# Optimization experiments

Hardware: AMD Instinct MI355X
Metric: run time of the kernel (lower is better)

## Reference

```python
import jax, jax.numpy as jnp
import numpy as np

N = 100000          # nodes
E = 1600000         # edges
D_IN = 128
HID = 256
N_CLASSES = 10
N_GRAPHS = 64


def gcn_conv(x, src, dst, W, b, n_nodes):
    """PyG GCNConv: add self-loops, symmetric deg^{-1/2} normalization, x@W, scatter-add."""
    h = x @ W  # [N, out]
    loop = jnp.arange(n_nodes, dtype=src.dtype)
    src2 = jnp.concatenate([src, loop])
    dst2 = jnp.concatenate([dst, loop])
    deg = jax.ops.segment_sum(jnp.ones(src2.shape[0], x.dtype), dst2, num_segments=n_nodes)
    dinv = jax.lax.rsqrt(deg)  # deg >= 1 thanks to self-loops
    norm = dinv[src2] * dinv[dst2]  # [E+N]
    msg = norm[:, None] * h[src2]   # [E+N, out]
    return jax.ops.segment_sum(msg, dst2, num_segments=n_nodes) + b


def setup_inputs() -> dict:
    key = jax.random.key(0)
    ks = jax.random.split(key, 12)
    x = jax.random.normal(ks[0], (N, D_IN), dtype=jnp.float32)
    edge_index = jax.random.randint(ks[1], (2, E), 0, N, dtype=jnp.int64)
    batch = jnp.sort(jax.random.randint(ks[2], (N,), 0, N_GRAPHS, dtype=jnp.int64))
    def glorot(k, shape):
        lim = float(np.sqrt(6.0 / (shape[0] + shape[1])))
        return jax.random.uniform(k, shape, jnp.float32, -lim, lim)
    W1 = glorot(ks[3], (D_IN, HID));  b1 = jnp.zeros((HID,), jnp.float32)
    W2 = glorot(ks[4], (HID, HID));   b2 = jnp.zeros((HID,), jnp.float32)
    Wf1 = glorot(ks[5], (HID, HID));  bf1 = jnp.zeros((HID,), jnp.float32)
    Wf2 = glorot(ks[6], (HID, N_CLASSES)); bf2 = jnp.zeros((N_CLASSES,), jnp.float32)
    return {"x": x, "edge_index": edge_index, "batch": batch,
            "W1": W1, "b1": b1, "W2": W2, "b2": b2,
            "Wf1": Wf1, "bf1": bf1, "Wf2": Wf2, "bf2": bf2}


def reference(x, edge_index, batch, W1, b1, W2, b2, Wf1, bf1, Wf2, bf2):
    src, dst = edge_index[0], edge_index[1]
    h = jax.nn.relu(gcn_conv(x, src, dst, W1, b1, N))
    h = jax.nn.relu(gcn_conv(h, src, dst, W2, b2, N))
    # global mean pool over graph ids
    summed = jax.ops.segment_sum(h, batch, num_segments=N_GRAPHS)  # [G, HID]
    counts = jax.ops.segment_sum(jnp.ones((N,), h.dtype), batch, num_segments=N_GRAPHS)
    pooled = summed / jnp.maximum(counts, 1.0)[:, None]
    z = jax.nn.relu(pooled @ Wf1 + bf1)
    alpha = jax.nn.softplus(z @ Wf2 + bf2) + 0.001
    return alpha
```

## Files before the change

### kernel.cpp

```cpp
#include <hip/hip_runtime.h>
#include <math.h>

#define NN   100000
#define NE   1600000
#define DIN  128
#define HID  256
#define NG   64
#define NCLS 10

#define NBLK 128
#define EPB  (NE / NBLK)
#define NBUK 512
#define NPB  196
#define NHIST (NBUK * NBLK)
#define NBR  ((NN + 127) / 128)

using bf16x8 = __attribute__((ext_vector_type(8))) short;
using f32x4  = __attribute__((ext_vector_type(4))) float;
using f32x2  = __attribute__((ext_vector_type(2))) float;
using u32x2  = __attribute__((ext_vector_type(2))) unsigned int;

static __device__ __forceinline__ unsigned short f2bf(float f) {
    unsigned u = __float_as_uint(f);
    u += 0x7fff + ((u >> 16) & 1);
    return (unsigned short)(u >> 16);
}

static __device__ __forceinline__ unsigned char f32_to_fp8(float f) {
    float a = fminf(fabsf(f), 448.f);
    unsigned bits = __float_as_uint(a * 0x1p-120f);
    bits += 0x7ffff + ((bits >> 20) & 1);
    unsigned e4 = (bits >> 20) & 0x7f;
    return (unsigned char)(e4 | (f < 0.f ? 0x80u : 0u));
}
#if __has_builtin(__builtin_amdgcn_cvt_pk_f32_fp8)
#define HAVE_CVT_FP8 1
#endif
static __device__ __forceinline__ void fp8x4_to_f32(unsigned u, float* f) {
#ifdef HAVE_CVT_FP8
    f32x2 lo = __builtin_amdgcn_cvt_pk_f32_fp8((int)u, false);
    f32x2 hi = __builtin_amdgcn_cvt_pk_f32_fp8((int)u, true);
    f[0] = lo[0]; f[1] = lo[1]; f[2] = hi[0]; f[3] = hi[1];
#else
#pragma unroll
    for (int k = 0; k < 4; ++k) {
        unsigned b = (u >> (8 * k)) & 0xffu;
        unsigned bits = ((b & 0x80u) << 24) | ((b & 0x7fu) << 20);
        f[k] = __uint_as_float(bits) * 0x1p+120f;
    }
#endif
}
static __device__ __forceinline__ int4 fp8x8_to_bf16x8(unsigned lo, unsigned hi) {
    float f[8];
    fp8x4_to_f32(lo, f);
    fp8x4_to_f32(hi, f + 4);
    int4 r;
    r.x = (int)((__float_as_uint(f[0]) >> 16) | (__float_as_uint(f[1]) & 0xffff0000u));
    r.y = (int)((__float_as_uint(f[2]) >> 16) | (__float_as_uint(f[3]) & 0xffff0000u));
    r.z = (int)((__float_as_uint(f[4]) >> 16) | (__float_as_uint(f[5]) & 0xffff0000u));
    r.w = (int)((__float_as_uint(f[6]) >> 16) | (__float_as_uint(f[7]) & 0xffff0000u));
    return r;
}


__global__ __launch_bounds__(256) void k_hist(const int* __restrict__ dst,
                                              int* __restrict__ histg) {
    __shared__ int h[NBUK];
    const int t = threadIdx.x;
    for (int i = t; i < NBUK; i += 256) h[i] = 0;
    __syncthreads();
    const int e0 = blockIdx.x * EPB, e1 = e0 + EPB;
    for (int e = e0 + t; e < e1; e += 256)
        atomicAdd(&h[(unsigned)__builtin_nontemporal_load(&dst[e]) / NPB], 1);
    __syncthreads();
    for (int i = t; i < NBUK; i += 256)
        histg[i * NBLK + blockIdx.x] = h[i];
}

__global__ __launch_bounds__(256) void k_bsum2(const int* __restrict__ d,
                                               int* __restrict__ bsum) {
    __shared__ int sd[256];
    int t = threadIdx.x;
    const int4 v = *(const int4*)&d[blockIdx.x * 1024 + t * 4];
    sd[t] = v.x + v.y + v.z + v.w;
    __syncthreads();
    for (int off = 128; off > 0; off >>= 1) {
        if (t < off) sd[t] += sd[t + off];
        __syncthreads();
    }
    if (t == 0) bsum[blockIdx.x] = sd[0];
}

__global__ void k_scanb2(const int* __restrict__ bsum, int* __restrict__ boff,
                         const int* __restrict__ batch, float* __restrict__ countsf) {
    __shared__ int tmp[64];
    int t = threadIdx.x;
    int v = bsum[t];
    tmp[t] = v; __syncthreads();
    for (int off = 1; off < 64; off <<= 1) {
        int u = (t >= off) ? tmp[t - off] : 0;
        __syncthreads();
        tmp[t] += u;
        __syncthreads();
    }
    boff[t] = tmp[t] - v;
    int g = t;
    int lo = 0, hi = NN;
    while (lo < hi) { int mid = (lo + hi) >> 1; if (batch[mid] < g) lo = mid + 1; else hi = mid; }
    int lb = lo;
    lo = 0; hi = NN;
    while (lo < hi) { int mid = (lo + hi) >> 1; if (batch[mid] <= g) lo = mid + 1; else hi = mid; }
    countsf[g] = (float)(lo - lb);
}

__global__ __launch_bounds__(256) void k_offs2(int* __restrict__ d,
                                               const int* __restrict__ boff) {
    __shared__ int ts[256];
    int t = threadIdx.x;
    int base = blockIdx.x * 1024 + t * 4;
    int4 v = *(const int4*)&d[base];
    int s = v.x + v.y + v.z + v.w;
    ts[t] = s; __syncthreads();
    for (int off = 1; off < 256; off <<= 1) {
        int u = (t >= off) ? ts[t - off] : 0;
        __syncthreads();
        ts[t] += u;
        __syncthreads();
    }
    int run = ts[t] - s + boff[blockIdx.x];
    int4 o;
    o.x = run; run += v.x;
    o.y = run; run += v.y;
    o.z = run; run += v.z;
    o.w = run; run += v.w;
    *(int4*)&d[base] = o;
}

__global__ __launch_bounds__(256) void k_scatter(const int* __restrict__ src,
                                                 const int* __restrict__ dst,
                                                 const int* __restrict__ offg,
                                                 unsigned* __restrict__ pairs) {
    __shared__ int cur[NBUK];
    const int t = threadIdx.x;
    for (int i = t; i < NBUK; i += 256) cur[i] = offg[i * NBLK + blockIdx.x];
    __syncthreads();
    const int e0 = blockIdx.x * EPB, e1 = e0 + EPB;
    for (int e = e0 + t; e < e1; e += 256) {
        int d = __builtin_nontemporal_load(&dst[e]);
        int sv = __builtin_nontemporal_load(&src[e]);
        int b = (unsigned)d / NPB;
        int li = d - b * NPB;
        unsigned pk = ((unsigned)li << 24) | (unsigned)sv;
        int p = atomicAdd(&cur[b], 1);
        __builtin_nontemporal_store(pk, &pairs[p]);
    }
}

__global__ __launch_bounds__(256) void k_csr(const unsigned* __restrict__ pairs,
                                             const int* __restrict__ offg,
                                             int* __restrict__ csr,
                                             int* __restrict__ deg,
                                             float* __restrict__ dinv,
                                             int* __restrict__ offs) {
    __shared__ int cnt[NPB];
    __shared__ int loff[256];
    __shared__ int cur[NPB];
    const int b = blockIdx.x, t = threadIdx.x;
    const int s     = offg[b * NBLK];
    const int e_end = (b == NBUK - 1) ? NE : offg[(b + 1) * NBLK];
    const int nb0   = b * NPB;
    const int nnod  = min(NPB, NN - nb0);
    if (t < NPB) cnt[t] = 0;
    __syncthreads();
    for (int e = s + t; e < e_end; e += 256)
        atomicAdd(&cnt[pairs[e] >> 24], 1);
    __syncthreads();
    int v = (t < NPB) ? cnt[t] : 0;
    loff[t] = v;
    __syncthreads();
    for (int off = 1; off < 256; off <<= 1) {
        int u = (t >= off) ? loff[t - off] : 0;
        __syncthreads();
        loff[t] += u;
        __syncthreads();
    }
    int myoff = loff[t] - v;
    __syncthreads();
    loff[t] = myoff;
    if (t < NPB) cur[t] = 0;
    __syncthreads();
    if (t < nnod) {
        int node = nb0 + t;
        int dg = cnt[t];
        deg[node]  = dg;
        dinv[node] = rsqrtf((float)(dg + 1));
        offs[node] = s + myoff;
    }
    for (int e = s + t; e < e_end; e += 256) {
        unsigned pk = pairs[e];
        int li = pk >> 24;
        int p = atomicAdd(&cur[li], 1);
        csr[s + loff[li] + p] = (int)(pk & 0xffffffu);
    }
}


#define XQ (NN * 32)

__global__ void k_cast_all(const float* __restrict__ x, const float* __restrict__ dinv,
                           unsigned char* __restrict__ xs8,
                           const float* __restrict__ W1, unsigned short* __restrict__ Wt1,
                           const float* __restrict__ W2, unsigned short* __restrict__ Wt2) {
    int i = blockIdx.x * blockDim.x + threadIdx.x;
    if (i < XQ) {
        int nd = i >> 5;
        int q  = i & 31;
        float dv = dinv[nd];
        const float4 v = *(const float4*)&x[(size_t)nd * DIN + q * 4];
        uchar4 o;
        o.x = f32_to_fp8(v.x * dv); o.y = f32_to_fp8(v.y * dv);
        o.z = f32_to_fp8(v.z * dv); o.w = f32_to_fp8(v.w * dv);
        *(uchar4*)&xs8[(size_t)nd * DIN + q * 4] = o;
        return;
    }
    int j = i - XQ;
    if (j < DIN * HID) {
        int k = j >> 8, nc = j & 255;
        Wt1[nc * DIN + k] = f2bf(W1[j]);
    } else if (j < (DIN + HID) * HID) {
        int jj = j - DIN * HID;
        int k = jj >> 8, nc = jj & 255;
        Wt2[nc * HID + k] = f2bf(W2[jj]);
    }
}


template <int MODE>
__global__ __launch_bounds__(256) void k_gemm_mfma(const unsigned char* __restrict__ A8,
                                                   const unsigned short* __restrict__ Wt,
                                                   const float* __restrict__ dinv,
                                                   const float* __restrict__ bias,
                                                   void* __restrict__ outp,
                                                   const int* __restrict__ batch,
                                                   int M, int K) {
    __shared__ unsigned short As[128 * 40];
    __shared__ unsigned short Bs[128 * 40];
    __shared__ float psum[4][128];
    __shared__ int gloc[128];
    const int t = threadIdx.x;
    const int lane = t & 63;
    const int wid = t >> 6;
    const int wr = wid >> 1, wc = wid & 1;
    const int bm = blockIdx.x * 128, bn = blockIdx.y * 128;
    const int lr = lane & 15;
    const int ko = (lane >> 4) << 3;

    f32x4 acc[4][4] = {};

    const int r = t >> 2;
    const int kq = (t & 3) << 3;

    int g0 = 0, gend = 0;
    if (MODE == 2) {
        g0 = batch[bm];
        gend = batch[min(bm + 127, M - 1)];
        for (int i = t; i < 4 * 128; i += 256) ((float*)psum)[i] = 0.f;
        if (t < 128) gloc[t] = (bm + t < M) ? min(batch[bm + t] - g0, 3) : 0;
    }

    for (int kk = 0; kk < K; kk += 32) {
#pragma unroll
        for (int h = 0; h < 128; h += 64) {
            int row = bm + r + h;
            int4 o = make_int4(0, 0, 0, 0);
            if (row < M) {
                u32x2 v = *(const u32x2*)&A8[(size_t)row * K + kk + kq];
                o = fp8x8_to_bf16x8(v.x, v.y);
            }
            *(int4*)&As[(r + h) * 40 + kq] = o;
        }
#pragma unroll
        for (int h = 0; h < 128; h += 64) {
            int nrow = bn + r + h;
            int4 v = *(const int4*)&Wt[(size_t)nrow * K + kk + kq];
            *(int4*)&Bs[(r + h) * 40 + kq] = v;
        }
        __syncthreads();
        bf16x8 af[4], bfr[4];
#pragma unroll
        for (int mf = 0; mf < 4; ++mf)
            af[mf] = *(const bf16x8*)&As[(wr * 64 + mf * 16 + lr) * 40 + ko];
#pragma unroll
        for (int nf = 0; nf < 4; ++nf)
            bfr[nf] = *(const bf16x8*)&Bs[(wc * 64 + nf * 16 + lr) * 40 + ko];
#pragma unroll
        for (int mf = 0; mf < 4; ++mf)
#pragma unroll
            for (int nf = 0; nf < 4; ++nf)
                acc[mf][nf] = __builtin_amdgcn_mfma_f32_16x16x32_bf16(af[mf], bfr[nf], acc[mf][nf], 0, 0, 0);
        __syncthreads();
    }

    if (MODE == 1) {
        unsigned char* out8 = (unsigned char*)outp;
#pragma unroll
        for (int mf = 0; mf < 4; ++mf) {
#pragma unroll
            for (int b = 0; b < 4; ++b) {
                int row = bm + wr * 64 + mf * 16 + (lane >> 4) * 4 + b;
                if (row >= M) continue;
                float dv = dinv[row];
#pragma unroll
                for (int nf = 0; nf < 4; ++nf) {
                    int col = bn + wc * 64 + nf * 16 + lr;
                    float v = fmaxf(acc[mf][nf][b] + bias[col], 0.f);
                    out8[(size_t)row * HID + col] = f32_to_fp8(dv * v);
                }
            }
        }
    } else {
        const int q4 = (lane >> 4) << 2;
        if (gend == g0) {
#pragma unroll
            for (int nf = 0; nf < 4; ++nf) {
                const int lcol = wc * 64 + nf * 16 + lr;
                const float bb = bias[bn + lcol];
                float rsum = 0.f;
#pragma unroll
                for (int mf = 0; mf < 4; ++mf)
#pragma unroll
                    for (int b = 0; b < 4; ++b) {
                        int lrow = wr * 64 + mf * 16 + q4 + b;
                        if (bm + lrow < M) rsum += fmaxf(acc[mf][nf][b] + bb, 0.f);
                    }
                rsum += __shfl_xor(rsum, 16);
                rsum += __shfl_xor(rsum, 32);
                if ((lane >> 4) == 0) atomicAdd(&psum[0][lcol], rsum);
            }
        } else {
#pragma unroll
            for (int nf = 0; nf < 4; ++nf) {
                const int lcol = wc * 64 + nf * 16 + lr;
                const float bb = bias[bn + lcol];
                float run = 0.f; int gcur = 0;
#pragma unroll
                for (int mf = 0; mf < 4; ++mf) {
#pragma unroll
                    for (int b = 0; b < 4; ++b) {
                        int lrow = wr * 64 + mf * 16 + q4 + b;
                        if (bm + lrow < M) {
                            int gl = gloc[lrow];
                            float v = fmaxf(acc[mf][nf][b] + bb, 0.f);
                            if (gl != gcur) {
                                if (run != 0.f) atomicAdd(&psum[gcur][lcol], run);
                                run = 0.f; gcur = gl;
                            }
                            run += v;
                        }
                    }
                }
                if (run != 0.f) atomicAdd(&psum[gcur][lcol], run);
            }
        }
        __syncthreads();
        float* scratch = (float*)outp;
        size_t base = ((size_t)blockIdx.x * 2 + blockIdx.y) * 512;
        for (int i = t; i < 512; i += 256)
            __builtin_nontemporal_store(((const float*)psum)[i], &scratch[base + i]);
    }
}


__global__ __launch_bounds__(128) void k_reduce(const float* __restrict__ scratch,
                                                const int* __restrict__ batch,
                                                float* __restrict__ pooled) {
    const int g = blockIdx.x >> 1, by = blockIdx.x & 1;
    const int t = threadIdx.x;
    int lo = 0, hi = NN;
    while (lo < hi) { int mid = (lo + hi) >> 1; if (batch[mid] < g) lo = mid + 1; else hi = mid; }
    int s = lo;
    lo = s; hi = NN;
    while (lo < hi) { int mid = (lo + hi) >> 1; if (batch[mid] <= g) lo = mid + 1; else hi = mid; }
    int e = lo;
    float sum = 0.f;
    if (e > s) {
        int bx0 = s >> 7, bx1 = (e - 1) >> 7;
        for (int bx = bx0; bx <= bx1; ++bx) {
            int gl = min(g - batch[bx << 7], 3);
            sum += scratch[((size_t)bx * 2 + by) * 512 + gl * 128 + t];
        }
    }
    pooled[g * HID + by * 128 + t] = sum;
}


__global__ __launch_bounds__(256) void k_agg256(const unsigned char* __restrict__ hs,
                                                const int* __restrict__ csr,
                                                const int* __restrict__ offs,
                                                const int* __restrict__ deg,
                                                const float* __restrict__ dinv,
                                                unsigned char* __restrict__ out, int n) {
    int wid = threadIdx.x >> 6, lane = threadIdx.x & 63;
    int node = blockIdx.x * 4 + wid;
    if (node >= n) return;
    int c = lane << 2;
    float a0, a1, a2, a3;
    {
        unsigned u = *(const unsigned*)&hs[(size_t)node * HID + c];
        float f[4]; fp8x4_to_f32(u, f);
        a0 = f[0]; a1 = f[1]; a2 = f[2]; a3 = f[3];
    }
    int s0 = offs[node], cnt = deg[node];
    for (int base = 0; base < cnt; base += 64) {
        int nb = min(64, cnt - base);
        int idx = (lane < nb) ? __builtin_nontemporal_load(&csr[s0 + base + lane]) : 0;
        int i = 0;
        for (; i + 8 <= nb; i += 8) {
            unsigned v[8];
#pragma unroll
            for (int k = 0; k < 8; ++k) {
                int j = __shfl(idx, i + k);
                v[k] = *(const unsigned*)&hs[(size_t)j * HID + c];
            }
#pragma unroll
            for (int k = 0; k < 8; ++k) {
                float f[4]; fp8x4_to_f32(v[k], f);
                a0 += f[0]; a1 += f[1]; a2 += f[2]; a3 += f[3];
            }
        }
        for (; i + 4 <= nb; i += 4) {
            unsigned v[4];
#pragma unroll
            for (int k = 0; k < 4; ++k) {
                int j = __shfl(idx, i + k);
                v[k] = *(const unsigned*)&hs[(size_t)j * HID + c];
            }
#pragma unroll
            for (int k = 0; k < 4; ++k) {
                float f[4]; fp8x4_to_f32(v[k], f);
                a0 += f[0]; a1 += f[1]; a2 += f[2]; a3 += f[3];
            }
        }
        for (; i < nb; ++i) {
            int j = __shfl(idx, i);
            unsigned u = *(const unsigned*)&hs[(size_t)j * HID + c];
            float f[4]; fp8x4_to_f32(u, f);
            a0 += f[0]; a1 += f[1]; a2 += f[2]; a3 += f[3];
        }
    }
    float dv = dinv[node];
    uchar4 r;
    r.x = f32_to_fp8(dv * a0); r.y = f32_to_fp8(dv * a1);
    r.z = f32_to_fp8(dv * a2); r.w = f32_to_fp8(dv * a3);
    *(uchar4*)&out[(size_t)node * HID + c] = r;
}


__global__ __launch_bounds__(256) void k_agg128(const unsigned char* __restrict__ xs,
                                                const int* __restrict__ csr,
                                                const int* __restrict__ offs,
                                                const int* __restrict__ deg,
                                                const float* __restrict__ dinv,
                                                unsigned char* __restrict__ out, int n) {
    int wid = threadIdx.x >> 6, lane = threadIdx.x & 63;
    int node = blockIdx.x * 4 + wid;
    if (node >= n) return;
    int half = lane >> 5, l32 = lane & 31;
    int c = l32 << 2;
    float a0 = 0.f, a1 = 0.f, a2 = 0.f, a3 = 0.f;
    if (half == 0) {
        unsigned u = *(const unsigned*)&xs[(size_t)node * DIN + c];
        float f[4]; fp8x4_to_f32(u, f);
        a0 = f[0]; a1 = f[1]; a2 = f[2]; a3 = f[3];
    }
    int s0 = offs[node], cnt = deg[node];
    for (int base = 0; base < cnt; base += 64) {
        int nb = min(64, cnt - base);
        int idx = (lane < nb) ? __builtin_nontemporal_load(&csr[s0 + base + lane]) : 0;
        int i = 0;
        for (; i + 8 <= nb; i += 8) {
            unsigned v[4];
#pragma unroll
            for (int k = 0; k < 4; ++k) {
                int j = __shfl(idx, i + 2 * k + half);
                v[k] = *(const unsigned*)&xs[(size_t)j * DIN + c];
            }
#pragma unroll
            for (int k = 0; k < 4; ++k) {
                float f[4]; fp8x4_to_f32(v[k], f);
                a0 += f[0]; a1 += f[1]; a2 += f[2]; a3 += f[3];
            }
        }
        for (; i < nb; i += 2) {
            int e = i + half;
            int j = __shfl(idx, e < nb ? e : 0);
            if (e < nb) {
                unsigned u = *(const unsigned*)&xs[(size_t)j * DIN + c];
                float f[4]; fp8x4_to_f32(u, f);
                a0 += f[0]; a1 += f[1]; a2 += f[2]; a3 += f[3];
            }
        }
    }
    a0 += __shfl_xor(a0, 32);
    a1 += __shfl_xor(a1, 32);
    a2 += __shfl_xor(a2, 32);
    a3 += __shfl_xor(a3, 32);
    if (half == 0) {
        float dv = dinv[node];
        uchar4 r;
        r.x = f32_to_fp8(dv * a0); r.y = f32_to_fp8(dv * a1);
        r.z = f32_to_fp8(dv * a2); r.w = f32_to_fp8(dv * a3);
        *(uchar4*)&out[(size_t)node * DIN + c] = r;
    }
}


__global__ __launch_bounds__(256) void k_mlp(const float* __restrict__ pooled,
                                             const float* __restrict__ countsf,
                                             const float* __restrict__ Wf1,
                                             const float* __restrict__ bf1,
                                             const float* __restrict__ Wf2,
                                             const float* __restrict__ bf2,
                                             float* __restrict__ out) {
    __shared__ float p[HID];
    __shared__ float z[HID];
    int g = blockIdx.x, t = threadIdx.x;
    float cnt = fmaxf(countsf[g], 1.0f);
    p[t] = pooled[g * HID + t] / cnt;
    __syncthreads();
    float accz = bf1[t];
    for (int k = 0; k < HID; ++k)
        accz = fmaf(p[k], Wf1[k * HID + t], accz);
    z[t] = fmaxf(accz, 0.f);
    __syncthreads();
    if (t < NCLS) {
        float o = bf2[t];
        for (int k = 0; k < HID; ++k)
            o = fmaf(z[k], Wf2[k * NCLS + t], o);
        float sp = fmaxf(o, 0.f) + log1pf(expf(-fabsf(o)));
        out[g * NCLS + t] = sp + 0.001f;
    }
}


extern "C" void kernel_launch(void* const* d_in, const int* in_sizes, int n_in,
                              void* d_out, int out_size, void* d_ws, size_t ws_size,
                              hipStream_t stream) {
    const float* x     = (const float*)d_in[0];
    const int*   ei    = (const int*)d_in[1];
    const int*   batch = (const int*)d_in[2];
    const float* W1    = (const float*)d_in[3];
    const float* b1    = (const float*)d_in[4];
    const float* W2    = (const float*)d_in[5];
    const float* b2    = (const float*)d_in[6];
    const float* Wf1   = (const float*)d_in[7];
    const float* bf1   = (const float*)d_in[8];
    const float* Wf2   = (const float*)d_in[9];
    const float* bf2   = (const float*)d_in[10];
    float* out = (float*)d_out;

    const int* srcv = ei;
    const int* dstv = ei + NE;

    char* p = (char*)d_ws;
    auto take = [&](size_t bytes) -> char* {
        char* q = p; p += (bytes + 255) & ~(size_t)255; return q;
    };
    char* big0 = take((size_t)NN * HID * 2);
    char* big1 = take((size_t)NN * HID * 2);
    unsigned char*  xs8 = (unsigned char*)big0;
    unsigned char*  xa8 = (unsigned char*)(big0 + (size_t)NN * DIN);
    unsigned char*  h8  = (unsigned char*)big1;
    unsigned char*  r8  = (unsigned char*)big0;
    float* scratch = (float*)(big1 + (size_t)NN * HID);
    unsigned* pairs = (unsigned*)big1;
    unsigned short* wt1  = (unsigned short*)take((size_t)DIN * HID * 2);
    unsigned short* wt2  = (unsigned short*)take((size_t)HID * HID * 2);
    int*   histg   = (int*)take((size_t)NHIST * 4);
    int*   bsum    = (int*)take(64 * 4);
    int*   boff    = (int*)take(64 * 4);
    int*   deg     = (int*)take((size_t)NN * 4);
    int*   offs    = (int*)take((size_t)NN * 4);
    int*   csr     = (int*)take((size_t)NE * 4);
    float* dinv    = (float*)take((size_t)NN * 4);
    float* pooled  = (float*)take((size_t)NG * HID * 4);
    float* countsf = (float*)take((size_t)NG * 4);

    k_hist<<<NBLK, 256, 0, stream>>>(dstv, histg);
    k_bsum2<<<64, 256, 0, stream>>>(histg, bsum);
    k_scanb2<<<1, 64, 0, stream>>>(bsum, boff, batch, countsf);
    k_offs2<<<64, 256, 0, stream>>>(histg, boff);
    k_scatter<<<NBLK, 256, 0, stream>>>(srcv, dstv, histg, pairs);
    k_csr<<<NBUK, 256, 0, stream>>>(pairs, histg, csr, deg, dinv, offs);

    int cast_total = XQ + (DIN + HID) * HID;
    k_cast_all<<<(cast_total + 255) / 256, 256, 0, stream>>>(x, dinv, xs8, W1, wt1, W2, wt2);

    dim3 gg(NBR, HID / 128);
    k_agg128<<<(NN + 3) / 4, 256, 0, stream>>>(xs8, csr, offs, deg, dinv, xa8, NN);
    k_gemm_mfma<1><<<gg, 256, 0, stream>>>(xa8, wt1, dinv, b1, (void*)h8, batch, NN, DIN);
    k_agg256<<<(NN + 3) / 4, 256, 0, stream>>>(h8, csr, offs, deg, dinv, r8, NN);
    k_gemm_mfma<2><<<gg, 256, 0, stream>>>(r8, wt2, dinv, b2, (void*)scratch, batch, NN, HID);
    k_reduce<<<2 * NG, 128, 0, stream>>>(scratch, batch, pooled);

    k_mlp<<<NG, 256, 0, stream>>>(pooled, countsf, Wf1, bf1, Wf2, bf2, out);
}
```

Baseline: 339.1 us.

## Widen GEMM block tile to full 256 columns with K-step 64

The GEMM block now covers 128 rows by all 256 output columns using 512 threads (8 waves), instead of two 128x128 blocks per row tile. The fp8 A tile is loaded and converted once per row block rather than twice, and the K loop steps by 64 with two MFMA sub-steps, halving the number of barriers. The pooled scratch layout is changed to 1024 floats per row block, and k_reduce is updated to match. This trades fewer blocks and more LDS per block (larger B tile) against lower occupancy.

```diff
diff --git a/kernel.cpp b/kernel.cpp
--- a/kernel.cpp
+++ b/kernel.cpp
@@ -19,6 +19,7 @@
 using f32x4  = __attribute__((ext_vector_type(4))) float;
 using f32x2  = __attribute__((ext_vector_type(2))) float;
 using u32x2  = __attribute__((ext_vector_type(2))) unsigned int;
+using u32x4  = __attribute__((ext_vector_type(4))) unsigned int;
 
 static __device__ __forceinline__ unsigned short f2bf(float f) {
     unsigned u = __float_as_uint(f);
@@ -236,68 +237,70 @@
 
 
 template <int MODE>
-__global__ __launch_bounds__(256) void k_gemm_mfma(const unsigned char* __restrict__ A8,
+__global__ __launch_bounds__(512) void k_gemm_mfma(const unsigned char* __restrict__ A8,
                                                    const unsigned short* __restrict__ Wt,
                                                    const float* __restrict__ dinv,
                                                    const float* __restrict__ bias,
                                                    void* __restrict__ outp,
                                                    const int* __restrict__ batch,
                                                    int M, int K) {
-    __shared__ unsigned short As[128 * 40];
-    __shared__ unsigned short Bs[128 * 40];
-    __shared__ float psum[4][128];
+    __shared__ unsigned short As[128 * 72];
+    __shared__ unsigned short Bs[256 * 72];
+    __shared__ float psum[4][256];
     __shared__ int gloc[128];
     const int t = threadIdx.x;
     const int lane = t & 63;
     const int wid = t >> 6;
-    const int wr = wid >> 1, wc = wid & 1;
-    const int bm = blockIdx.x * 128, bn = blockIdx.y * 128;
+    const int wr = wid & 1, wc = wid >> 1;
+    const int bm = blockIdx.x * 128;
     const int lr = lane & 15;
     const int ko = (lane >> 4) << 3;
 
     f32x4 acc[4][4] = {};
 
-    const int r = t >> 2;
-    const int kq = (t & 3) << 3;
+    const int arow = t >> 2;
+    const int akq  = (t & 3) << 4;
+    const int brow = t >> 1;
+    const int bkq  = (t & 1) << 5;
 
     int g0 = 0, gend = 0;
     if (MODE == 2) {
         g0 = batch[bm];
         gend = batch[min(bm + 127, M - 1)];
-        for (int i = t; i < 4 * 128; i += 256) ((float*)psum)[i] = 0.f;
+        for (int i = t; i < 4 * 256; i += 512) ((float*)psum)[i] = 0.f;
         if (t < 128) gloc[t] = (bm + t < M) ? min(batch[bm + t] - g0, 3) : 0;
     }
 
-    for (int kk = 0; kk < K; kk += 32) {
-#pragma unroll
-        for (int h = 0; h < 128; h += 64) {
-            int row = bm + r + h;
-            int4 o = make_int4(0, 0, 0, 0);
-            if (row < M) {
-                u32x2 v = *(const u32x2*)&A8[(size_t)row * K + kk + kq];
-                o = fp8x8_to_bf16x8(v.x, v.y);
-            }
-            *(int4*)&As[(r + h) * 40 + kq] = o;
-        }
-#pragma unroll
-        for (int h = 0; h < 128; h += 64) {
-            int nrow = bn + r + h;
-            int4 v = *(const int4*)&Wt[(size_t)nrow * K + kk + kq];
-            *(int4*)&Bs[(r + h) * 40 + kq] = v;
-        }
-        __syncthreads();
-        bf16x8 af[4], bfr[4];
-#pragma unroll
-        for (int mf = 0; mf < 4; ++mf)
-            af[mf] = *(const bf16x8*)&As[(wr * 64 + mf * 16 + lr) * 40 + ko];
-#pragma unroll
-        for (int nf = 0; nf < 4; ++nf)
-            bfr[nf] = *(const bf16x8*)&Bs[(wc * 64 + nf * 16 + lr) * 40 + ko];
-#pragma unroll
-        for (int mf = 0; mf < 4; ++mf)
+    for (int kk = 0; kk < K; kk += 64) {
+        {
+            int row = bm + arow;
+            u32x4 v; v.x = v.y = v.z = v.w = 0u;
+            if (row < M) v = *(const u32x4*)&A8[(size_t)row * K + kk + akq];
+            *(int4*)&As[arow * 72 + akq]     = fp8x8_to_bf16x8(v.x, v.y);
+            *(int4*)&As[arow * 72 + akq + 8] = fp8x8_to_bf16x8(v.z, v.w);
+        }
+        {
+            const unsigned short* wsrc = &Wt[(size_t)brow * K + kk + bkq];
+#pragma unroll
+            for (int q = 0; q < 4; ++q)
+                *(int4*)&Bs[brow * 72 + bkq + q * 8] = *(const int4*)&wsrc[q * 8];
+        }
+        __syncthreads();
+#pragma unroll
+        for (int ks = 0; ks < 64; ks += 32) {
+            bf16x8 af[4], bfr[4];
+#pragma unroll
+            for (int mf = 0; mf < 4; ++mf)
+                af[mf] = *(const bf16x8*)&As[(wr * 64 + mf * 16 + lr) * 72 + ks + ko];
 #pragma unroll
             for (int nf = 0; nf < 4; ++nf)
-                acc[mf][nf] = __builtin_amdgcn_mfma_f32_16x16x32_bf16(af[mf], bfr[nf], acc[mf][nf], 0, 0, 0);
+                bfr[nf] = *(const bf16x8*)&Bs[(wc * 64 + nf * 16 + lr) * 72 + ks + ko];
+#pragma unroll
+            for (int mf = 0; mf < 4; ++mf)
+#pragma unroll
+                for (int nf = 0; nf < 4; ++nf)
+                    acc[mf][nf] = __builtin_amdgcn_mfma_f32_16x16x32_bf16(af[mf], bfr[nf], acc[mf][nf], 0, 0, 0);
+        }
         __syncthreads();
     }
 
@@ -312,7 +315,7 @@
                 float dv = dinv[row];
 #pragma unroll
                 for (int nf = 0; nf < 4; ++nf) {
-                    int col = bn + wc * 64 + nf * 16 + lr;
+                    int col = wc * 64 + nf * 16 + lr;
                     float v = fmaxf(acc[mf][nf][b] + bias[col], 0.f);
                     out8[(size_t)row * HID + col] = f32_to_fp8(dv * v);
                 }
@@ -324,7 +327,7 @@
 #pragma unroll
             for (int nf = 0; nf < 4; ++nf) {
                 const int lcol = wc * 64 + nf * 16 + lr;
-                const float bb = bias[bn + lcol];
+                const float bb = bias[lcol];
                 float rsum = 0.f;
 #pragma unroll
                 for (int mf = 0; mf < 4; ++mf)
@@ -341,7 +344,7 @@
 #pragma unroll
             for (int nf = 0; nf < 4; ++nf) {
                 const int lcol = wc * 64 + nf * 16 + lr;
-                const float bb = bias[bn + lcol];
+                const float bb = bias[lcol];
                 float run = 0.f; int gcur = 0;
 #pragma unroll
                 for (int mf = 0; mf < 4; ++mf) {
@@ -364,8 +367,8 @@
         }
         __syncthreads();
         float* scratch = (float*)outp;
-        size_t base = ((size_t)blockIdx.x * 2 + blockIdx.y) * 512;
-        for (int i = t; i < 512; i += 256)
+        size_t base = (size_t)blockIdx.x * 1024;
+        for (int i = t; i < 1024; i += 512)
             __builtin_nontemporal_store(((const float*)psum)[i], &scratch[base + i]);
     }
 }
@@ -376,6 +379,7 @@
                                                 float* __restrict__ pooled) {
     const int g = blockIdx.x >> 1, by = blockIdx.x & 1;
     const int t = threadIdx.x;
+    const int col = by * 128 + t;
     int lo = 0, hi = NN;
     while (lo < hi) { int mid = (lo + hi) >> 1; if (batch[mid] < g) lo = mid + 1; else hi = mid; }
     int s = lo;
@@ -387,10 +391,10 @@
         int bx0 = s >> 7, bx1 = (e - 1) >> 7;
         for (int bx = bx0; bx <= bx1; ++bx) {
             int gl = min(g - batch[bx << 7], 3);
-            sum += scratch[((size_t)bx * 2 + by) * 512 + gl * 128 + t];
-        }
-    }
-    pooled[g * HID + by * 128 + t] = sum;
+            sum += scratch[(size_t)bx * 1024 + gl * 256 + col];
+        }
+    }
+    pooled[g * HID + col] = sum;
 }
 
 
@@ -596,11 +600,10 @@
     int cast_total = XQ + (DIN + HID) * HID;
     k_cast_all<<<(cast_total + 255) / 256, 256, 0, stream>>>(x, dinv, xs8, W1, wt1, W2, wt2);
 
-    dim3 gg(NBR, HID / 128);
     k_agg128<<<(NN + 3) / 4, 256, 0, stream>>>(xs8, csr, offs, deg, dinv, xa8, NN);
-    k_gemm_mfma<1><<<gg, 256, 0, stream>>>(xa8, wt1, dinv, b1, (void*)h8, batch, NN, DIN);
+    k_gemm_mfma<1><<<NBR, 512, 0, stream>>>(xa8, wt1, dinv, b1, (void*)h8, batch, NN, DIN);
     k_agg256<<<(NN + 3) / 4, 256, 0, stream>>>(h8, csr, offs, deg, dinv, r8, NN);
-    k_gemm_mfma<2><<<gg, 256, 0, stream>>>(r8, wt2, dinv, b2, (void*)scratch, batch, NN, HID);
+    k_gemm_mfma<2><<<NBR, 512, 0, stream>>>(r8, wt2, dinv, b2, (void*)scratch, batch, NN, HID);
     k_reduce<<<2 * NG, 128, 0, stream>>>(scratch, batch, pooled);
 
     k_mlp<<<NG, 256, 0, stream>>>(pooled, countsf, Wf1, bf1, Wf2, bf2, out);
```

Result: faster. 327.9 us (-3.3%).
